# Performance work log

Hardware: AMD Instinct MI355X
Metric: run time of the kernel (lower is better)

Reference implementation:

```python
import jax, jax.numpy as jnp
import numpy as np

B, L, E, C = 256, 1024, 128, 5  # trees, leaves per tree, embed size, num classes

def setup_inputs() -> dict:
    key = jax.random.key(0)
    k1, k2, k3 = jax.random.split(key, 3)
    leaves = jax.random.normal(k1, (B, L, E), dtype=jnp.float32)
    # Glorot-ish scaling so 10 stacked relu(Linear) levels stay well-conditioned
    W = jax.random.normal(k2, (E, 2 * E), dtype=jnp.float32) * (2.0 / (2 * E)) ** 0.5
    bW = jnp.zeros((E,), dtype=jnp.float32)
    P = jax.random.normal(k3, (C, E), dtype=jnp.float32) * (2.0 / E) ** 0.5
    bP = jnp.zeros((C,), dtype=jnp.float32)
    return {"leaves": leaves, "W": W, "bW": bW, "P": P, "bP": bP}

def reference(leaves, W, bW, P, bP):
    """Batched level-by-level bottom-up pass over a forest of perfect binary trees.
    Per internal node (same math as RecursiveNN.traverse):
        h = relu(W @ concat(left, right) + bW)
        proj = P @ h + bP
    Returns all internal-node projections concatenated: [B*(L-1), C].
    """
    x = leaves  # [B, n, E] current frontier of node embeddings
    probs = []
    while x.shape[1] > 1:
        # pair adjacent siblings: [B, n/2, 2E]
        pairs = jnp.concatenate([x[:, 0::2], x[:, 1::2]], axis=-1)
        h = jax.nn.relu(jnp.einsum('bnf,ef->bne', pairs, W) + bW)  # [B, n/2, E]
        proj = jnp.einsum('bne,ce->bnc', h, P) + bP                # [B, n/2, C]
        probs.append(proj.reshape(-1, P.shape[0]))
        x = h
    return jnp.concatenate(probs, axis=0)  # [B*(L-1), C]
```

## Files before the change

kernel.cpp:

```cpp
#include <hip/hip_runtime.h>
#include <hip/hip_bf16.h>
#include <hip/hip_fp16.h>


typedef _Float16 f16_t;
typedef _Float16 f16x4 __attribute__((ext_vector_type(4)));
typedef _Float16 f16x8 __attribute__((ext_vector_type(8)));
typedef float f32x4 __attribute__((ext_vector_type(4)));

#define HSTRIDE 136

static __device__ __forceinline__ f32x4 mfma16(f16x8 a, f16x8 b, f32x4 c) {
    return __builtin_amdgcn_mfma_f32_16x16x32_f16(a, b, c, 0, 0, 0);
}

__global__ void prep_kernel(const float* __restrict__ W, const float* __restrict__ P,
                            f16_t* __restrict__ Wh, f16_t* __restrict__ Ph) {
    if (blockIdx.x < 128) {
        const int i = blockIdx.x * 256 + threadIdx.x;
        Wh[i] = (f16_t)W[i];
    } else {
        for (int i = threadIdx.x; i < 640; i += 256) Ph[i] = (f16_t)P[i];
    }
}

__global__ __launch_bounds__(256, 2)
void forest_kernel(const float* __restrict__ leaves,
                   const f16_t* __restrict__ Wh,
                   const f16_t* __restrict__ Ph,
                   const float* __restrict__ bW,
                   const float* __restrict__ bP,
                   f16_t* __restrict__ Q,
                   float* __restrict__ out)
{
    __shared__ f16_t AR[128 * HSTRIDE];
    __shared__ f16_t HB2[32 * HSTRIDE];
    __shared__ float OutB[640];

    const int tid   = threadIdx.x;
    const int wave  = tid >> 6;
    const int lane  = tid & 63;
    const int mlane = lane & 15;
    const int q     = lane >> 4;
    const int tree  = blockIdx.x >> 3;
    const int e     = blockIdx.x & 7;
    const float* leafbase = leaves + (size_t)blockIdx.x * 16384;

    f16x8 wh[2][8];
    float bwv[2];
    #pragma unroll
    for (int n = 0; n < 2; ++n) {
        const int col = wave * 32 + n * 16 + mlane;
        bwv[n] = bW[col];
        #pragma unroll
        for (int k = 0; k < 8; ++k)
            wh[n][k] = *(const f16x8*)&Wh[col * 256 + k * 32 + q * 8];
    }

    f16x8 pb[4] = {};
    if (mlane < 5) {
        #pragma unroll
        for (int kb = 0; kb < 4; ++kb)
            pb[kb] = *(const f16x8*)&Ph[mlane * 128 + kb * 32 + q * 8];
    }
    const float bpv = (mlane < 5) ? bP[mlane] : 0.f;

    #pragma unroll
    for (int b = 0; b < 2; ++b) {
        float4 t[8];
        #pragma unroll
        for (int r = 0; r < 8; ++r)
            t[r] = ((const float4*)leafbase)[tid + (b * 8 + r) * 256];
        #pragma unroll
        for (int r = 0; r < 8; ++r) {
            const int idx = tid + (b * 8 + r) * 256;
            const int row = idx >> 5;
            const int c4  = idx & 31;
            f16x4 t4 = { (f16_t)t[r].x, (f16_t)t[r].y, (f16_t)t[r].z, (f16_t)t[r].w };
            *(f16x4*)&AR[row * HSTRIDE + c4 * 4] = t4;
        }
    }

    auto level_step = [&](const f16_t* src, f16_t* dst) {
        f16x8 af[8];
        #pragma unroll
        for (int k = 0; k < 8; ++k) {
            const int off  = k * 64 + q * 16;
            const int trow = off >> 8;
            const int ce   = (off & 255) >> 1;
            af[k] = *(const f16x8*)&src[(2 * mlane + trow) * HSTRIDE + ce];
        }
        f32x4 acc0 = {}, acc1 = {};
        #pragma unroll
        for (int k = 0; k < 8; ++k) {
            acc0 = mfma16(af[k], wh[0][k], acc0);
            acc1 = mfma16(af[k], wh[1][k], acc1);
        }
        #pragma unroll
        for (int r = 0; r < 4; ++r) {
            float v0 = fmaxf(acc0[r] + bwv[0], 0.f);
            float v1 = fmaxf(acc1[r] + bwv[1], 0.f);
            dst[(q * 4 + r) * HSTRIDE + wave * 32 + mlane]      = (f16_t)v0;
            dst[(q * 4 + r) * HSTRIDE + wave * 32 + 16 + mlane] = (f16_t)v1;
        }
    };

    auto proj_to_outb = [&](const f16_t* hb, int orow0, int valid) {
        f32x4 pc = {};
        #pragma unroll
        for (int kb = 0; kb < 4; ++kb) {
            const f16x8 ha = *(const f16x8*)&hb[mlane * HSTRIDE + kb * 32 + q * 8];
            pc = mfma16(ha, pb[kb], pc);
        }
        if (mlane < 5) {
            #pragma unroll
            for (int r = 0; r < 4; ++r) {
                const int row = q * 4 + r;
                if (row < valid) OutB[(orow0 + row) * 5 + mlane] = pc[r] + bpv;
            }
        }
    };

    __syncthreads();

    level_step(&AR[ 0 * HSTRIDE], &HB2[ 0 * HSTRIDE]);
    level_step(&AR[32 * HSTRIDE], &HB2[16 * HSTRIDE]);
    __syncthreads();
    level_step(&AR[64 * HSTRIDE], &AR[ 0 * HSTRIDE]);
    level_step(&AR[96 * HSTRIDE], &AR[16 * HSTRIDE]);
    __syncthreads();

    {
        const f16_t* pbase = (wave < 2) ? &HB2[(wave * 16) * HSTRIDE]
                                        : &AR[((wave - 2) * 16) * HSTRIDE];
        proj_to_outb(pbase, wave * 16, 16);
    }

    level_step(&HB2[0 * HSTRIDE], &AR[32 * HSTRIDE]);
    level_step(&AR [0 * HSTRIDE], &AR[48 * HSTRIDE]);
    __syncthreads();
    if (wave == 0) proj_to_outb(&AR[32 * HSTRIDE], 64, 16);
    if (wave == 1) proj_to_outb(&AR[48 * HSTRIDE], 80, 16);

    level_step(&AR[32 * HSTRIDE], &AR[0 * HSTRIDE]);
    __syncthreads();
    if (wave == 2) proj_to_outb(&AR[0 * HSTRIDE], 96, 16);

    level_step(&AR[0 * HSTRIDE], &AR[16 * HSTRIDE]);
    __syncthreads();
    if (wave == 3) proj_to_outb(&AR[16 * HSTRIDE], 112, 8);

    level_step(&AR[16 * HSTRIDE], &AR[24 * HSTRIDE]);
    __syncthreads();
    if (wave == 0) proj_to_outb(&AR[24 * HSTRIDE], 120, 4);

    level_step(&AR[24 * HSTRIDE], &AR[28 * HSTRIDE]);
    __syncthreads();
    if (wave == 1) proj_to_outb(&AR[28 * HSTRIDE], 124, 2);

    level_step(&AR[28 * HSTRIDE], &AR[30 * HSTRIDE]);
    __syncthreads();
    if (wave == 2) proj_to_outb(&AR[30 * HSTRIDE], 126, 1);
    __syncthreads();

    for (int t2 = tid; t2 < 635; t2 += 256) {
        const int lrow = t2 / 5;
        const int cls  = t2 - lrow * 5;
        int j, i;
        if      (lrow <  64) { j = 1; i = lrow;       }
        else if (lrow <  96) { j = 2; i = lrow - 64;  }
        else if (lrow < 112) { j = 3; i = lrow - 96;  }
        else if (lrow < 120) { j = 4; i = lrow - 112; }
        else if (lrow < 124) { j = 5; i = lrow - 120; }
        else if (lrow < 126) { j = 6; i = lrow - 124; }
        else                 { j = 7; i = 0;          }
        const size_t grow = (size_t)256 * (1024 - (2048 >> j))
                          + (size_t)tree * (1024 >> j) + (size_t)e * (128 >> j) + i;
        out[grow * 5 + cls] = OutB[t2];
    }

    if (tid < 16)
        *(uint4*)&Q[(size_t)blockIdx.x * 128 + tid * 8] = *(const uint4*)&AR[30 * HSTRIDE + tid * 8];
}

__global__ __launch_bounds__(128, 4)
void rnn_top_kernel(const f16_t* __restrict__ Q,
                    const float* __restrict__ W,
                    const float* __restrict__ bW,
                    const float* __restrict__ P,
                    const float* __restrict__ bP,
                    float* __restrict__ out)
{
    __shared__ float qs[1024];
    __shared__ float hs[896];
    const int t    = threadIdx.x;
    const int tree = blockIdx.x;

    #pragma unroll
    for (int i = 0; i < 8; ++i)
        qs[t + i * 128] = (float)Q[(size_t)tree * 1024 + t + i * 128];
    __syncthreads();

    const float* wr = W + t * 256;

    float s8[4];
    #pragma unroll
    for (int n = 0; n < 4; ++n) s8[n] = bW[t];
    for (int k = 0; k < 256; k += 4) {
        const float4 wv = *(const float4*)(wr + k);
        #pragma unroll
        for (int n = 0; n < 4; ++n) {
            const float* qb = qs + n * 256 + k;
            s8[n] += wv.x * qb[0] + wv.y * qb[1] + wv.z * qb[2] + wv.w * qb[3];
        }
    }
    #pragma unroll
    for (int n = 0; n < 4; ++n) hs[n * 128 + t] = fmaxf(s8[n], 0.f);
    __syncthreads();

    float s9[2];
    s9[0] = s9[1] = bW[t];
    for (int k = 0; k < 256; k += 4) {
        const float4 wv = *(const float4*)(wr + k);
        #pragma unroll
        for (int m = 0; m < 2; ++m) {
            const float* hb = hs + m * 256 + k;
            s9[m] += wv.x * hb[0] + wv.y * hb[1] + wv.z * hb[2] + wv.w * hb[3];
        }
    }
    hs[512 + t] = fmaxf(s9[0], 0.f);
    hs[640 + t] = fmaxf(s9[1], 0.f);
    __syncthreads();

    float s10 = bW[t];
    for (int k = 0; k < 256; k += 4) {
        const float4 wv = *(const float4*)(wr + k);
        const float* hb = hs + 512 + k;
        s10 += wv.x * hb[0] + wv.y * hb[1] + wv.z * hb[2] + wv.w * hb[3];
    }
    hs[768 + t] = fmaxf(s10, 0.f);
    __syncthreads();

    if (t < 35) {
        const int node = t / 5, c = t % 5;
        float s = bP[c];
        const float* hb = hs + node * 128;
        for (int k = 0; k < 128; ++k) s += hb[k] * P[c * 128 + k];
        size_t row;
        if (node < 4)      row = 260096 + (size_t)tree * 4 + node;
        else if (node < 6) row = 261120 + (size_t)tree * 2 + (node - 4);
        else               row = 261632 + (size_t)tree;
        out[row * 5 + c] = s;
    }
}

extern "C" void kernel_launch(void* const* d_in, const int* in_sizes, int n_in,
                              void* d_out, int out_size, void* d_ws, size_t ws_size,
                              hipStream_t stream) {
    const float* leaves = (const float*)d_in[0];
    const float* W      = (const float*)d_in[1];
    const float* bW     = (const float*)d_in[2];
    const float* P      = (const float*)d_in[3];
    const float* bP     = (const float*)d_in[4];
    float* out = (float*)d_out;

    f16_t* Wh = (f16_t*)d_ws;
    f16_t* Ph = Wh + 32768;
    f16_t* Q  = Wh + 32768 + 1024;

    prep_kernel<<<dim3(129), dim3(256), 0, stream>>>(W, P, Wh, Ph);
    forest_kernel<<<dim3(2048), dim3(256), 0, stream>>>(leaves, Wh, Ph, bW, bP, Q, out);
    rnn_top_kernel<<<dim3(256), dim3(128), 0, stream>>>(Q, W, bW, P, bP, out);
}
```

Before: 225.2 us.

## Drop HB2 scratch buffer, reuse AR in place, split MFMA accumulator chains

Removes the separate HB2 LDS buffer. The first level now reads its fragments into registers, synchronises, then writes results in place into AR, and later levels ping-pong between two regions of AR. This shrinks LDS per block, which may allow more blocks per CU. The MFMA accumulations for both the level step and the projection are split into two independent chains that are summed at the end, which shortens dependency latency. The cost is extra barriers inside the first-level loop and a few more accumulator registers.

```diff
diff --git a/kernel.cpp b/kernel.cpp
--- a/kernel.cpp
+++ b/kernel.cpp
@@ -34,7 +34,6 @@
                    float* __restrict__ out)
 {
     __shared__ f16_t AR[128 * HSTRIDE];
-    __shared__ f16_t HB2[32 * HSTRIDE];
     __shared__ float OutB[640];
 
     const int tid   = threadIdx.x;
@@ -81,8 +80,7 @@
         }
     }
 
-    auto level_step = [&](const f16_t* src, f16_t* dst) {
-        f16x8 af[8];
+    auto read_frags = [&](const f16_t* src, f16x8* af) {
         #pragma unroll
         for (int k = 0; k < 8; ++k) {
             const int off  = k * 64 + q * 16;
@@ -90,77 +88,91 @@
             const int ce   = (off & 255) >> 1;
             af[k] = *(const f16x8*)&src[(2 * mlane + trow) * HSTRIDE + ce];
         }
-        f32x4 acc0 = {}, acc1 = {};
-        #pragma unroll
-        for (int k = 0; k < 8; ++k) {
-            acc0 = mfma16(af[k], wh[0][k], acc0);
-            acc1 = mfma16(af[k], wh[1][k], acc1);
+    };
+    auto mfma_write = [&](const f16x8* af, f16_t* dst) {
+        f32x4 a0 = {}, b0 = {}, a1 = {}, b1 = {};
+        #pragma unroll
+        for (int k = 0; k < 4; ++k) {
+            a0 = mfma16(af[k], wh[0][k], a0);
+            a1 = mfma16(af[k], wh[1][k], a1);
+        }
+        #pragma unroll
+        for (int k = 4; k < 8; ++k) {
+            b0 = mfma16(af[k], wh[0][k], b0);
+            b1 = mfma16(af[k], wh[1][k], b1);
         }
         #pragma unroll
         for (int r = 0; r < 4; ++r) {
-            float v0 = fmaxf(acc0[r] + bwv[0], 0.f);
-            float v1 = fmaxf(acc1[r] + bwv[1], 0.f);
+            float v0 = fmaxf(a0[r] + b0[r] + bwv[0], 0.f);
+            float v1 = fmaxf(a1[r] + b1[r] + bwv[1], 0.f);
             dst[(q * 4 + r) * HSTRIDE + wave * 32 + mlane]      = (f16_t)v0;
             dst[(q * 4 + r) * HSTRIDE + wave * 32 + 16 + mlane] = (f16_t)v1;
         }
     };
-
     auto proj_to_outb = [&](const f16_t* hb, int orow0, int valid) {
-        f32x4 pc = {};
-        #pragma unroll
-        for (int kb = 0; kb < 4; ++kb) {
-            const f16x8 ha = *(const f16x8*)&hb[mlane * HSTRIDE + kb * 32 + q * 8];
-            pc = mfma16(ha, pb[kb], pc);
+        f32x4 p0 = {}, p1 = {};
+        {
+            const f16x8 h0 = *(const f16x8*)&hb[mlane * HSTRIDE + 0 * 32 + q * 8];
+            const f16x8 h1 = *(const f16x8*)&hb[mlane * HSTRIDE + 1 * 32 + q * 8];
+            const f16x8 h2 = *(const f16x8*)&hb[mlane * HSTRIDE + 2 * 32 + q * 8];
+            const f16x8 h3 = *(const f16x8*)&hb[mlane * HSTRIDE + 3 * 32 + q * 8];
+            p0 = mfma16(h0, pb[0], p0); p1 = mfma16(h1, pb[1], p1);
+            p0 = mfma16(h2, pb[2], p0); p1 = mfma16(h3, pb[3], p1);
         }
         if (mlane < 5) {
             #pragma unroll
             for (int r = 0; r < 4; ++r) {
                 const int row = q * 4 + r;
-                if (row < valid) OutB[(orow0 + row) * 5 + mlane] = pc[r] + bpv;
+                if (row < valid) OutB[(orow0 + row) * 5 + mlane] = p0[r] + p1[r] + bpv;
             }
         }
     };
 
     __syncthreads();
 
-    level_step(&AR[ 0 * HSTRIDE], &HB2[ 0 * HSTRIDE]);
-    level_step(&AR[32 * HSTRIDE], &HB2[16 * HSTRIDE]);
-    __syncthreads();
-    level_step(&AR[64 * HSTRIDE], &AR[ 0 * HSTRIDE]);
-    level_step(&AR[96 * HSTRIDE], &AR[16 * HSTRIDE]);
-    __syncthreads();
-
+    #pragma unroll
+    for (int c = 0; c < 4; ++c) {
+        f16x8 af[8];
+        read_frags(&AR[(32 * c) * HSTRIDE], af);
+        __syncthreads();
+        mfma_write(af, &AR[(16 * c) * HSTRIDE]);
+    }
+    __syncthreads();
+
+    proj_to_outb(&AR[(16 * wave) * HSTRIDE], 16 * wave, 16);
     {
-        const f16_t* pbase = (wave < 2) ? &HB2[(wave * 16) * HSTRIDE]
-                                        : &AR[((wave - 2) * 16) * HSTRIDE];
-        proj_to_outb(pbase, wave * 16, 16);
-    }
-
-    level_step(&HB2[0 * HSTRIDE], &AR[32 * HSTRIDE]);
-    level_step(&AR [0 * HSTRIDE], &AR[48 * HSTRIDE]);
-    __syncthreads();
-    if (wave == 0) proj_to_outb(&AR[32 * HSTRIDE], 64, 16);
-    if (wave == 1) proj_to_outb(&AR[48 * HSTRIDE], 80, 16);
-
-    level_step(&AR[32 * HSTRIDE], &AR[0 * HSTRIDE]);
-    __syncthreads();
-    if (wave == 2) proj_to_outb(&AR[0 * HSTRIDE], 96, 16);
-
-    level_step(&AR[0 * HSTRIDE], &AR[16 * HSTRIDE]);
-    __syncthreads();
-    if (wave == 3) proj_to_outb(&AR[16 * HSTRIDE], 112, 8);
-
-    level_step(&AR[16 * HSTRIDE], &AR[24 * HSTRIDE]);
-    __syncthreads();
-    if (wave == 0) proj_to_outb(&AR[24 * HSTRIDE], 120, 4);
-
-    level_step(&AR[24 * HSTRIDE], &AR[28 * HSTRIDE]);
-    __syncthreads();
-    if (wave == 1) proj_to_outb(&AR[28 * HSTRIDE], 124, 2);
-
-    level_step(&AR[28 * HSTRIDE], &AR[30 * HSTRIDE]);
-    __syncthreads();
-    if (wave == 2) proj_to_outb(&AR[30 * HSTRIDE], 126, 1);
+        f16x8 af[8];
+        read_frags(&AR[0], af);
+        mfma_write(af, &AR[64 * HSTRIDE]);
+        read_frags(&AR[32 * HSTRIDE], af);
+        mfma_write(af, &AR[80 * HSTRIDE]);
+    }
+    __syncthreads();
+
+    if (wave == 0) proj_to_outb(&AR[64 * HSTRIDE], 64, 16);
+    if (wave == 1) proj_to_outb(&AR[80 * HSTRIDE], 80, 16);
+    { f16x8 af[8]; read_frags(&AR[64 * HSTRIDE], af); mfma_write(af, &AR[0]); }
+    __syncthreads();
+
+    if (wave == 2) proj_to_outb(&AR[0], 96, 16);
+    { f16x8 af[8]; read_frags(&AR[0], af); mfma_write(af, &AR[32 * HSTRIDE]); }
+    __syncthreads();
+
+    if (wave == 3) proj_to_outb(&AR[32 * HSTRIDE], 112, 8);
+    { f16x8 af[8]; read_frags(&AR[32 * HSTRIDE], af); mfma_write(af, &AR[0]); }
+    __syncthreads();
+
+    if (wave == 0) proj_to_outb(&AR[0], 120, 4);
+    { f16x8 af[8]; read_frags(&AR[0], af); mfma_write(af, &AR[32 * HSTRIDE]); }
+    __syncthreads();
+
+    if (wave == 1) proj_to_outb(&AR[32 * HSTRIDE], 124, 2);
+    { f16x8 af[8]; read_frags(&AR[32 * HSTRIDE], af); mfma_write(af, &AR[0]); }
+    __syncthreads();
+
+    if (wave == 2) proj_to_outb(&AR[0], 126, 1);
+    if (tid < 16)
+        *(uint4*)&Q[(size_t)blockIdx.x * 128 + tid * 8] = *(const uint4*)&AR[tid * 8];
     __syncthreads();
 
     for (int t2 = tid; t2 < 635; t2 += 256) {
@@ -178,9 +190,6 @@
                           + (size_t)tree * (1024 >> j) + (size_t)e * (128 >> j) + i;
         out[grow * 5 + cls] = OutB[t2];
     }
-
-    if (tid < 16)
-        *(uint4*)&Q[(size_t)blockIdx.x * 128 + tid * 8] = *(const uint4*)&AR[30 * HSTRIDE + tid * 8];
 }
 
 __global__ __launch_bounds__(128, 4)
```

Result: faster. 220.5 us (-2.1%).
